# Optimization experiments

Measured on AMD Instinct MI355X. Metric: run time of the kernel, lower is better.

The kernel has to match this reference:

```python
import jax, jax.numpy as jnp
from jax import lax
import numpy as np

B, C, T = 32, 62, 1024
SR = 256
NUM_T = 32
POOL, STEP = 16, 4
OUT_G, POOL_G = 64, 32
NUM_CLASS = 4
KS = [int(0.1 * SR), int(0.2 * SR), int(0.5 * SR)]  # 25, 51, 128
EPS = 1e-30

def _feat_size():
    total = 0
    for k in KS:
        L = T - k + 1
        total += (L - POOL) // STEP + 1
    return NUM_T * (total // 2)  # AvgPool(1,2) halves the concat length

F_DIM = _feat_size()  # 32 * 354 = 11328


def setup_inputs() -> dict:
    key = jax.random.key(0)
    ks = jax.random.split(key, 32)
    n = lambda i, shape, s=0.05: jax.random.normal(ks[i], shape, dtype=jnp.float32) * s
    return dict(
        x=jax.random.normal(ks[0], (B, 1, C, T), dtype=jnp.float32),
        conv1_w=n(1, (NUM_T, 1, 1, KS[0])), conv1_b=jnp.zeros((NUM_T,), jnp.float32),
        conv2_w=n(2, (NUM_T, 1, 1, KS[1])), conv2_b=jnp.zeros((NUM_T,), jnp.float32),
        conv3_w=n(3, (NUM_T, 1, 1, KS[2])), conv3_b=jnp.zeros((NUM_T,), jnp.float32),
        oxo_w=n(4, (NUM_T, NUM_T)), oxo_b=jnp.zeros((NUM_T,), jnp.float32),
        lf_w=n(5, (C, F_DIM), 1.0), lf_b=jnp.zeros((1, C, 1), jnp.float32),
        global_adj=n(6, (C, C), 1.0),
        entry_w=n(7, (F_DIM, OUT_G)), entry_b=jnp.zeros((1, 1, OUT_G), jnp.float32),
        pool_w=n(8, (F_DIM, POOL_G)), pool_b=jnp.zeros((1, 1, POOL_G), jnp.float32),
        pl_w=n(9, (POOL_G, POOL_G), 0.1), pl_b=jnp.zeros((POOL_G,), jnp.float32),
        embed_w=n(10, (OUT_G, OUT_G), 0.1), embed_b=jnp.zeros((1, 1, OUT_G), jnp.float32),
        fc1_w=n(11, (2 * OUT_G, 2 * OUT_G), 0.1), fc1_b=jnp.zeros((2 * OUT_G,), jnp.float32),
        fc2_w=n(12, (2 * OUT_G, OUT_G), 0.1), fc2_b=jnp.zeros((OUT_G,), jnp.float32),
        fc3_w=n(13, (OUT_G, NUM_CLASS), 0.1), fc3_b=jnp.zeros((NUM_CLASS,), jnp.float32),
    )


def _bn(t, axes, eps=1e-5):
    # training-mode batchnorm with gamma=1, beta=0 (init values)
    m = t.mean(axes, keepdims=True)
    v = t.var(axes, keepdims=True)
    return (t - m) / jnp.sqrt(v + eps)


def _temporal(x, w, b):
    # Conv2d(1, NUM_T, (1,k)) -> square -> AvgPool(1,POOL) stride (1,STEP) -> log
    y = lax.conv_general_dilated(x, w, (1, 1), 'VALID',
                                 dimension_numbers=('NCHW', 'OIHW', 'NCHW'))
    y = y + b[None, :, None, None]
    y = y * y
    y = lax.reduce_window(y, 0.0, lax.add, (1, 1, 1, POOL), (1, 1, 1, STEP), 'VALID') / POOL
    return jnp.log(y)


def _forward(x, conv1_w, conv1_b, conv2_w, conv2_b, conv3_w, conv3_b, oxo_w, oxo_b,
             lf_w, lf_b, global_adj, entry_w, entry_b, pool_w, pool_b, pl_w, pl_b,
             embed_w, embed_b, fc1_w, fc1_b, fc2_w, fc2_b, fc3_w, fc3_b):
    # temporal branches, concat along time
    out = jnp.concatenate([_temporal(x, conv1_w, conv1_b),
                           _temporal(x, conv2_w, conv2_b),
                           _temporal(x, conv3_w, conv3_b)], axis=-1)  # [B,NUM_T,C,Lt]
    out = _bn(out, (0, 2, 3))  # BN_t
    # OneXOneConv: dropout(eval)=id, 1x1 conv, leaky_relu, AvgPool(1,2)
    out = jnp.einsum('bchw,oc->bohw', out, oxo_w) + oxo_b[None, :, None, None]
    out = jnp.where(out > 0, out, 0.01 * out)
    out = lax.reduce_window(out, 0.0, lax.add, (1, 1, 1, 2), (1, 1, 1, 2), 'VALID') / 2.0
    out = _bn(out, (0, 2, 3))  # BN_t_
    # [B,NUM_T,C,L] -> [B,C,NUM_T*L]
    out = jnp.transpose(out, (0, 2, 1, 3)).reshape(out.shape[0], C, -1)
    # local_filter_fun + apply_bn
    out = jax.nn.relu(out * lf_w[None] - lf_b)
    out = _bn(out, (0, 2))
    # get_adj: self-similarity, learned global adj, self loops, sym normalization
    s = jnp.einsum('bnf,bmf->bnm', out, out)
    adj = jax.nn.relu(s * (global_adj + global_adj.T)) + jnp.eye(C, dtype=out.dtype)
    rowsum = adj.sum(-1)
    rowsum = jnp.where(rowsum == 0, rowsum + 1.0, rowsum)
    d = rowsum ** -0.5
    adj = adj * d[:, :, None] * d[:, None, :]
    # entry GCN + bn_ + attention pooling (softmax over last dim of size 1 -> ones)
    h_entry = _bn(jnp.einsum('bnm,bmf->bnf', adj, out) @ entry_w - entry_b, (0, 2))
    tg1 = jnp.tanh(h_entry.mean(1))
    sc1 = jax.nn.softmax(jnp.einsum('bnf,bf->bn', h_entry, tg1)[..., None], axis=-1)
    rep1 = jnp.einsum('bnf,bn->bf', h_entry, sc1[..., 0])
    # pool GCN -> assignment
    h_pool = _bn(jnp.einsum('bnm,bmf->bnf', adj, out) @ pool_w - pool_b, (0, 2))
    s_assign = jax.nn.softmax(h_pool @ pl_w + pl_b, axis=-1)  # [B,C,POOL_G]
    # dense_diff_pool
    x_pool = jnp.einsum('bnk,bnf->bkf', s_assign, h_entry)
    adj_pool = jnp.einsum('bnk,bnm,bml->bkl', s_assign, adj, s_assign)
    link = adj - jnp.einsum('bnk,bmk->bnm', s_assign, s_assign) + EPS
    link_loss = jnp.linalg.norm(link.reshape(-1)) / adj.size
    ent_loss = (-s_assign * jnp.log(s_assign + EPS)).sum(-1).mean()
    # embed GCN + apply_bn + attention pooling
    h = _bn(jnp.einsum('bkl,blf->bkf', adj_pool, x_pool) @ embed_w - embed_b, (0, 2))
    tg2 = jnp.tanh(h.mean(1))
    sc2 = jax.nn.softmax(jnp.einsum('bkf,bf->bk', h, tg2)[..., None], axis=-1)
    rep2 = jnp.einsum('bkf,bk->bf', h, sc2[..., 0])
    # head
    o = jnp.concatenate([rep1, rep2], axis=1)
    o = jax.nn.relu(o @ fc1_w + fc1_b)
    o = jax.nn.relu(o @ fc2_w + fc2_b)
    o = o @ fc3_w + fc3_b
    o = _bn(o, (0,))  # apply_bn on [B, num_class]
    return o, link_loss, ent_loss


def reference(x, conv1_w, conv1_b, conv2_w, conv2_b, conv3_w, conv3_b, oxo_w, oxo_b,
              lf_w, lf_b, global_adj, entry_w, entry_b, pool_w, pool_b, pl_w, pl_b,
              embed_w, embed_b, fc1_w, fc1_b, fc2_w, fc2_b, fc3_w, fc3_b):
    return _forward(x, conv1_w, conv1_b, conv2_w, conv2_b, conv3_w, conv3_b, oxo_w, oxo_b,
                    lf_w, lf_b, global_adj, entry_w, entry_b, pool_w, pool_b, pl_w, pl_b,
                    embed_w, embed_b, fc1_w, fc1_b, fc2_w, fc2_b, fc3_w, fc3_b)
```

## Files before the change

### kernel.cpp

```cpp
#include <hip/hip_runtime.h>
#include <math.h>

typedef float  f32x4 __attribute__((ext_vector_type(4)));
typedef short  s16x4 __attribute__((ext_vector_type(4)));
typedef short  s16x8 __attribute__((ext_vector_type(8)));

constexpr int cB  = 32;
constexpr int cC  = 62;
constexpr int cT  = 1024;
constexpr int cNT = 32;
constexpr int cLT = 708;
constexpr int cLT2= 354;
constexpr int cFD = 11328;
constexpr int cNBC = cB*cC;

constexpr size_t FEAT_N = (size_t)cB*cNT*cC*cLT;
constexpr size_t P_N    = (size_t)cB*cC*cC;
constexpr size_t Q_N    = (size_t)cB*cC*96;
constexpr size_t R_N    = (size_t)cB*64;
constexpr size_t PART_N = (size_t)cNBC*64;
constexpr size_t ADJ_N  = P_N;
constexpr size_t HE_N   = (size_t)cB*cC*64;
constexpr size_t HP_N   = (size_t)cB*cC*32;
constexpr size_t HPRE_N = (size_t)cB*32*64;
constexpr int WBF_N = 32*32 + 32*64 + 32*128;
constexpr size_t WT_N = (size_t)96*cFD;

__device__ __forceinline__ unsigned short bf16rne(float v){
  unsigned int u = __float_as_uint(v);
  unsigned int r = (u + 0x7fffu + ((u>>16)&1u)) >> 16;
  return (unsigned short)r;
}

__global__ __launch_bounds__(256) void k_prep(
    const float* __restrict__ w1, const float* __restrict__ w2,
    const float* __restrict__ w3, const float* __restrict__ entry_w,
    const float* __restrict__ pool_w,
    unsigned short* __restrict__ wH, unsigned short* __restrict__ wL,
    float* __restrict__ wcol,
    unsigned short* __restrict__ WTH, unsigned short* __restrict__ WTL)
{
  int blk = blockIdx.x, tid = threadIdx.x;
  if (blk < 28){
    int i = blk*256 + tid;
    float v;
    if (i < 1024){ int f=i>>5, k=i&31; v = (k<25) ? w1[f*25+k] : 0.f; }
    else if (i < 3072){ int j=i-1024; int f=j>>6, k=j&63; v = (k<51) ? w2[f*51+k] : 0.f; }
    else { v = w3[i-3072]; }
    unsigned short h = bf16rne(v);
    float hf = __uint_as_float(((unsigned int)h)<<16);
    wH[i] = h;
    wL[i] = bf16rne(v - hf);
  } else {
    int j = blk - 28;
    float s = 0.f;
    for (int k=tid;k<cFD;k+=256){
      float v = (j<64) ? entry_w[(size_t)k*64 + j] : pool_w[(size_t)k*32 + (j-64)];
      s += v;
      unsigned short h = bf16rne(v);
      float hf = __uint_as_float(((unsigned int)h)<<16);
      WTH[(size_t)j*cFD + k] = h;
      WTL[(size_t)j*cFD + k] = bf16rne(v - hf);
    }
    __shared__ float red[256];
    red[tid]=s; __syncthreads();
    for (int o=128;o>0;o>>=1){ if(tid<o) red[tid]+=red[tid+o]; __syncthreads(); }
    if (tid==0) wcol[j] = red[0];
  }
}

template<int KS, int MT, int WOFF>
__device__ __forceinline__ void mfma_branch(
    const unsigned short* xH, const unsigned short* xL,
    const unsigned short* __restrict__ wHg, const unsigned short* __restrict__ wLg,
    const float* __restrict__ biasg, float* pt, int tid)
{
  int lane = tid & 63, wv = tid >> 6;
  int f = lane & 15, q = lane >> 4;
  int s = lane & 3;
  int a12 = lane & 12;
  s16x8 BH[2][KS], BL[2][KS];
  #pragma unroll
  for (int nt=0; nt<2; nt++)
    #pragma unroll
    for (int ks=0; ks<KS; ks++){
      size_t wo = (size_t)WOFF + (size_t)(nt*16+f)*(KS*32) + ks*32 + q*8;
      BH[nt][ks] = *(const s16x8*)&wHg[wo];
      BL[nt][ks] = *(const s16x8*)&wLg[wo];
    }
  float bv0 = biasg[f], bv1 = biasg[16+f];
  for (int mt = wv; mt < MT; mt += 4){
    f32x4 acc0 = {0.f,0.f,0.f,0.f};
    f32x4 acc1 = {0.f,0.f,0.f,0.f};
    int e0 = mt*16 + a12;
    #pragma unroll
    for (int ks=0; ks<KS; ks++){
      int e = e0 + q*8 + ks*32;
      const unsigned short* ph = xH + s*1160 + e;
      const unsigned short* pl = xL + s*1160 + e;
      s16x4 h0 = *(const s16x4*)ph;
      s16x4 h1 = *(const s16x4*)(ph+4);
      s16x4 l0 = *(const s16x4*)pl;
      s16x4 l1 = *(const s16x4*)(pl+4);
      s16x8 Ah = __builtin_shufflevector(h0,h1,0,1,2,3,4,5,6,7);
      s16x8 Al = __builtin_shufflevector(l0,l1,0,1,2,3,4,5,6,7);
      acc0 = __builtin_amdgcn_mfma_f32_16x16x32_bf16(Ah, BH[0][ks], acc0, 0,0,0);
      acc0 = __builtin_amdgcn_mfma_f32_16x16x32_bf16(Ah, BL[0][ks], acc0, 0,0,0);
      acc0 = __builtin_amdgcn_mfma_f32_16x16x32_bf16(Al, BH[0][ks], acc0, 0,0,0);
      acc1 = __builtin_amdgcn_mfma_f32_16x16x32_bf16(Ah, BH[1][ks], acc1, 0,0,0);
      acc1 = __builtin_amdgcn_mfma_f32_16x16x32_bf16(Ah, BL[1][ks], acc1, 0,0,0);
      acc1 = __builtin_amdgcn_mfma_f32_16x16x32_bf16(Al, BH[1][ks], acc1, 0,0,0);
    }
    float p0=0.f, p1=0.f;
    #pragma unroll
    for (int r=0;r<4;r++){
      float t0 = acc0[r]+bv0; p0 = fmaf(t0,t0,p0);
      float t1 = acc1[r]+bv1; p1 = fmaf(t1,t1,p1);
    }
    pt[(size_t)f*261      + mt*4 + q] = p0;
    pt[(size_t)(16+f)*261 + mt*4 + q] = p1;
  }
}

template<int P, int OFF>
__device__ __forceinline__ void pool_phase(
    const float* pt, float* __restrict__ feat, size_t rstr, size_t base_bc,
    float* tsum, float* tsq, int tid)
{
  bool act = tid < P;
  for (int fi=0; fi<32; fi++){
    float lv = 0.f;
    if (act){
      const float* pp = &pt[(size_t)fi*261 + tid];
      float pooled = (pp[0]+pp[1]+pp[2]+pp[3])*(1.f/16.f);
      lv = __logf(pooled);
      feat[base_bc + (size_t)fi*rstr + OFF + tid] = lv;
    }
    float v = lv, qq = lv*lv;
    #pragma unroll
    for (int o=32;o>0;o>>=1){ v += __shfl_down(v,o,64); qq += __shfl_down(qq,o,64); }
    if ((tid&63)==0){ atomicAdd(&tsum[fi], v); atomicAdd(&tsq[fi], qq); }
  }
}

__global__ __launch_bounds__(256) void k_conv(
    const float* __restrict__ x,
    const unsigned short* __restrict__ wH, const unsigned short* __restrict__ wL,
    const float* __restrict__ b1, const float* __restrict__ b2, const float* __restrict__ b3,
    float* __restrict__ feat, float* __restrict__ part1)
{
  __shared__ unsigned short xH[4*1160];
  __shared__ unsigned short xL[4*1160];
  __shared__ float pt[32*261];
  __shared__ float tsum[32], tsq[32];
  int b = blockIdx.x / cC, c = blockIdx.x % cC;
  int tid = threadIdx.x;
  const float* xg = x + (size_t)(b*cC+c)*cT;
  if (tid<32){ tsum[tid]=0.f; tsq[tid]=0.f; }
  for (int i=tid; i<4*1160; i+=256){
    int s = i / 1160, idx = i - s*1160;
    int src = idx + s;
    float v = (src < 1024) ? xg[src] : 0.f;
    unsigned short h = bf16rne(v);
    float hf = __uint_as_float(((unsigned int)h)<<16);
    xH[i] = h;
    xL[i] = bf16rne(v - hf);
  }
  size_t base_bc = ((size_t)(b*cNT)*cC + c)*cLT;
  size_t rstr = (size_t)cC*cLT;
  __syncthreads();
  mfma_branch<1,63,0>(xH,xL,wH,wL,b1,pt,tid);
  __syncthreads();
  pool_phase<247,0>(pt,feat,rstr,base_bc,tsum,tsq,tid);
  __syncthreads();
  mfma_branch<2,61,1024>(xH,xL,wH,wL,b2,pt,tid);
  __syncthreads();
  pool_phase<240,247>(pt,feat,rstr,base_bc,tsum,tsq,tid);
  __syncthreads();
  mfma_branch<4,57,3072>(xH,xL,wH,wL,b3,pt,tid);
  __syncthreads();
  pool_phase<221,487>(pt,feat,rstr,base_bc,tsum,tsq,tid);
  __syncthreads();
  if (tid<32){
    part1[(size_t)blockIdx.x*64 + tid*2]   = tsum[tid];
    part1[(size_t)blockIdx.x*64 + tid*2+1] = tsq[tid];
  }
}

__global__ __launch_bounds__(256) void k_reduce_stats(
    const float* __restrict__ part, double* __restrict__ stat, int nblk, int nch)
{
  int ch = blockIdx.x, tid = threadIdx.x;
  double s=0,q=0;
  for (int i=tid;i<nblk;i+=256){
    s += (double)part[(size_t)i*nch*2 + ch*2];
    q += (double)part[(size_t)i*nch*2 + ch*2 + 1];
  }
  __shared__ double ls[256], lq[256];
  ls[tid]=s; lq[tid]=q; __syncthreads();
  for (int o=128;o>0;o>>=1){ if(tid<o){ls[tid]+=ls[tid+o]; lq[tid]+=lq[tid+o];} __syncthreads(); }
  if (tid==0){ stat[ch*2]=ls[0]; stat[ch*2+1]=lq[0]; }
}

__global__ void k_foldw(const double* __restrict__ stat1,
                        const float* __restrict__ oxo_w, const float* __restrict__ oxo_b,
                        float* __restrict__ W2T, float* __restrict__ Cf)
{
  __shared__ float mu[32], inv[32];
  int tid = threadIdx.x;
  if (tid<32){
    double cnt = (double)cB*cC*cLT;
    double m = stat1[tid*2]/cnt;
    double v = stat1[tid*2+1]/cnt - m*m;
    mu[tid] = (float)m; inv[tid] = (float)(1.0/sqrt(v+1e-5));
  }
  __syncthreads();
  for (int i=tid;i<1024;i+=256){
    int t=i>>5, o=i&31;
    W2T[t*32+o] = oxo_w[o*32+t]*inv[t];
  }
  if (tid<32){
    float cacc = oxo_b[tid];
    for (int t=0;t<32;t++) cacc -= oxo_w[tid*32+t]*inv[t]*mu[t];
    Cf[tid] = cacc;
  }
}

__global__ __launch_bounds__(256) void k_mix(
    float* __restrict__ feat, const float* __restrict__ W2T,
    const float* __restrict__ Cf, float* __restrict__ part2)
{
  __shared__ float ft[32*240];
  __shared__ float wLh[1024];
  __shared__ float cL[32];
  int b = blockIdx.x / cC, c = blockIdx.x % cC;
  int tid = threadIdx.x;
  int lane = tid & 63, oset = (tid>>6)*8;
  for (int i=tid;i<1024;i+=256) wLh[i] = W2T[i];
  if (tid<32) cL[tid] = Cf[tid];
  float sacc[8]={0,0,0,0,0,0,0,0}, qacc[8]={0,0,0,0,0,0,0,0};
  for (int ch=0; ch<3; ch++){
    int l0 = ch*236;
    __syncthreads();
    for (int g=tid; g<32*59; g+=256){
      int t = g/59, l4 = (g - t*59)*4;
      *(float4*)&ft[t*240+l4] = *(const float4*)&feat[((size_t)(b*cNT+t)*cC + c)*cLT + l0 + l4];
    }
    __syncthreads();
    if (lane < 59){
      float m[8][4];
      #pragma unroll
      for (int f=0;f<8;f++){ float cv=cL[oset+f]; m[f][0]=cv;m[f][1]=cv;m[f][2]=cv;m[f][3]=cv; }
      #pragma unroll 4
      for (int t=0;t<32;t++){
        float4 z = *(const float4*)&ft[t*240 + 4*lane];
        float4 wa = *(const float4*)&wLh[t*32+oset];
        float4 wb = *(const float4*)&wLh[t*32+oset+4];
        float w8a[8] = {wa.x,wa.y,wa.z,wa.w, wb.x,wb.y,wb.z,wb.w};
        #pragma unroll
        for (int f=0;f<8;f++){
          m[f][0]=fmaf(z.x,w8a[f],m[f][0]);
          m[f][1]=fmaf(z.y,w8a[f],m[f][1]);
          m[f][2]=fmaf(z.z,w8a[f],m[f][2]);
          m[f][3]=fmaf(z.w,w8a[f],m[f][3]);
        }
      }
      #pragma unroll
      for (int f=0;f<8;f++){
        float a0 = m[f][0]>0.f ? m[f][0] : 0.01f*m[f][0];
        float a1 = m[f][1]>0.f ? m[f][1] : 0.01f*m[f][1];
        float a2 = m[f][2]>0.f ? m[f][2] : 0.01f*m[f][2];
        float a3 = m[f][3]>0.f ? m[f][3] : 0.01f*m[f][3];
        float v0 = 0.5f*(a0+a1), v1 = 0.5f*(a2+a3);
        float2 st; st.x=v0; st.y=v1;
        *(float2*)&feat[((size_t)(b*cNT+oset+f)*cC + c)*cLT + 118*ch + 2*lane] = st;
        sacc[f] += v0+v1; qacc[f] += v0*v0+v1*v1;
      }
    }
  }
  #pragma unroll
  for (int f=0;f<8;f++){
    float s = sacc[f], q = qacc[f];
    #pragma unroll
    for (int o=32;o>0;o>>=1){ s += __shfl_down(s,o,64); q += __shfl_down(q,o,64); }
    if (lane==0){
      part2[(size_t)blockIdx.x*64 + (oset+f)*2]   = s;
      part2[(size_t)blockIdx.x*64 + (oset+f)*2+1] = q;
    }
  }
}

__global__ __launch_bounds__(256) void k_vprep(
    float* __restrict__ feat, const double* __restrict__ stat2,
    const float* __restrict__ lf_w, const float* __restrict__ lf_b,
    float* __restrict__ r_g, float* __restrict__ SQb)
{
  __shared__ float a_s[32], b_s[32];
  __shared__ float red[256], red2[256];
  int b = blockIdx.x / cC, c = blockIdx.x % cC;
  int tid = threadIdx.x;
  if (tid<32){
    double cnt = (double)cB*cC*cLT2;
    double m = stat2[tid*2]/cnt;
    double v = stat2[tid*2+1]/cnt - m*m;
    float inv = (float)(1.0/sqrt(v+1e-5));
    a_s[tid] = inv;
    b_s[tid] = -(float)m*inv;
  }
  __syncthreads();
  float lb = lf_b[c];
  float S=0.f, SQ=0.f;
  unsigned* featU = (unsigned*)feat;
  for (int i=tid;i<cFD;i+=256){
    int t = i/cLT2, l2 = i - t*cLT2;
    size_t ad = ((size_t)(b*cNT+t)*cC + c)*cLT + l2;
    float raw = feat[ad];
    float z = fmaf(raw, a_s[t], b_s[t]);
    float v = fmaxf(fmaf(z, lf_w[(size_t)c*cFD + i], -lb), 0.f);
    S += v; SQ = fmaf(v,v,SQ);
    unsigned short h = bf16rne(v);
    float hf = __uint_as_float(((unsigned int)h)<<16);
    unsigned short lo = bf16rne(v - hf);
    featU[ad] = (((unsigned)h)<<16) | (unsigned)lo;
  }
  red[tid]=S; red2[tid]=SQ; __syncthreads();
  for (int o=128;o>0;o>>=1){ if(tid<o){red[tid]+=red[tid+o]; red2[tid]+=red2[tid+o];} __syncthreads(); }
  if (tid==0){ r_g[b*64+c]=red[0]; SQb[b*64+c]=red2[0]; }
}

__global__ __launch_bounds__(256) void k_gram(
    const unsigned* __restrict__ featP,
    const unsigned short* __restrict__ WTH, const unsigned short* __restrict__ WTL,
    float* __restrict__ P, float* __restrict__ Q)
{
  __shared__ unsigned short VH[64*72];
  __shared__ unsigned short VL[64*72];
  __shared__ unsigned short WH[96*72];
  __shared__ unsigned short WL[96*72];
  int b = blockIdx.x >> 4, ks = blockIdx.x & 15;
  int tid = threadIdx.x;
  int lane = tid & 63, wv = tid >> 6;
  int cn = lane & 15, q = lane >> 4;
  int nts[3]; int nnt = 0;
  for (int t = wv; t < 10; t += 4) nts[nnt++] = t;
  f32x4 acc[4][3];
  #pragma unroll
  for (int mt=0;mt<4;mt++)
    #pragma unroll
    for (int j=0;j<3;j++) acc[mt][j] = (f32x4){0.f,0.f,0.f,0.f};

  int t0 = (ks*64)/cLT2;
  int l20 = ks*64 - t0*cLT2;
  for (int chunk = ks; chunk < 177; chunk += 16){
    __syncthreads();
    for (int i=tid; i<62*64; i+=256){
      int n = i>>6, k = i&63;
      int fl = l20 + k;
      int cross = (fl >= cLT2);
      int t = t0 + cross;
      int l2 = fl - (cross ? cLT2 : 0);
      unsigned w = featP[((size_t)(b*cNT+t)*cC + n)*cLT + l2];
      VH[n*72+k] = (unsigned short)(w>>16);
      VL[n*72+k] = (unsigned short)(w & 0xffffu);
    }
    {
      int k0 = chunk*64;
      for (int i=tid; i<96*64; i+=256){
        int n = i>>6, k = i&63;
        WH[n*72+k] = WTH[(size_t)n*cFD + k0 + k];
        WL[n*72+k] = WTL[(size_t)n*cFD + k0 + k];
      }
    }
    __syncthreads();
    #pragma unroll
    for (int kst=0;kst<2;kst++){
      s16x8 AH[4], AL[4];
      #pragma unroll
      for (int mt=0;mt<4;mt++){
        AH[mt] = *(const s16x8*)&VH[(mt*16+cn)*72 + kst*32 + q*8];
        AL[mt] = *(const s16x8*)&VL[(mt*16+cn)*72 + kst*32 + q*8];
      }
      for (int j=0;j<nnt;j++){
        int nt = nts[j];
        s16x8 BH, BL;
        if (nt < 4){
          BH = *(const s16x8*)&VH[(nt*16+cn)*72 + kst*32 + q*8];
          BL = *(const s16x8*)&VL[(nt*16+cn)*72 + kst*32 + q*8];
        } else {
          BH = *(const s16x8*)&WH[((nt-4)*16+cn)*72 + kst*32 + q*8];
          BL = *(const s16x8*)&WL[((nt-4)*16+cn)*72 + kst*32 + q*8];
        }
        #pragma unroll
        for (int mt=0;mt<4;mt++){
          acc[mt][j] = __builtin_amdgcn_mfma_f32_16x16x32_bf16(AH[mt], BH, acc[mt][j],0,0,0);
          acc[mt][j] = __builtin_amdgcn_mfma_f32_16x16x32_bf16(AH[mt], BL, acc[mt][j],0,0,0);
          acc[mt][j] = __builtin_amdgcn_mfma_f32_16x16x32_bf16(AL[mt], BH, acc[mt][j],0,0,0);
        }
      }
    }
    l20 += 1024;
    while (l20 >= cLT2){ l20 -= cLT2; t0++; }
  }
  for (int j=0;j<nnt;j++){
    int nt = nts[j];
    for (int mt=0;mt<4;mt++){
      #pragma unroll
      for (int r=0;r<4;r++){
        int m = mt*16 + q*4 + r;
        if (m >= 62) continue;
        float v = acc[mt][j][r];
        if (nt < 4){
          int n = nt*16 + cn;
          if (n < 62) atomicAdd(&P[((size_t)b*cC+m)*cC + n], v);
        } else {
          int jn = (nt-4)*16 + cn;
          atomicAdd(&Q[((size_t)b*cC+m)*96 + jn], v);
        }
      }
    }
  }
}

__global__ __launch_bounds__(256) void k_adjgcn(
    const float* __restrict__ P, const float* __restrict__ r_g,
    const float* __restrict__ SQb,
    const float* __restrict__ gadj, const float* __restrict__ Q,
    const float* __restrict__ wcol,
    const float* __restrict__ entry_b, const float* __restrict__ pool_b,
    float* __restrict__ adj, float* __restrict__ hE, float* __restrict__ hP,
    double* __restrict__ statE, double* __restrict__ statP)
{
  __shared__ float a[3844];
  __shared__ float oL[5952];
  __shared__ float dsh[62];
  __shared__ float rL[62], mL[62], iL[62], wcL[96];
  __shared__ float es[62], eq[62], ps[62], pq[62];
  int b = blockIdx.x, tid = threadIdx.x;
  if (tid<62){
    double S=0, SQ=0;
    for (int b2=0;b2<32;b2++){
      S  += (double)r_g[(size_t)b2*64 + tid];
      SQ += (double)SQb[(size_t)b2*64 + tid];
    }
    double cnt = (double)cB*cFD;
    double m = S/cnt, var = SQ/cnt - m*m;
    mL[tid] = (float)m;
    iL[tid] = (float)(1.0/sqrt(var+1e-5));
    rL[tid] = r_g[(size_t)b*64+tid];
    es[tid]=0.f; eq[tid]=0.f; ps[tid]=0.f; pq[tid]=0.f;
  }
  if (tid>=64 && tid<160) wcL[tid-64]=wcol[tid-64];
  __syncthreads();
  for (int i=tid;i<3844;i+=256){
    int n=i/62, m=i-n*62;
    float sv = (P[(size_t)b*3844+i] - mL[n]*rL[m] - mL[m]*rL[n] + (float)cFD*mL[n]*mL[m]) * iL[n]*iL[m];
    float g = gadj[n*62+m] + gadj[m*62+n];
    float v = sv*g;
    v = v>0.f ? v : 0.f;
    if (n==m) v += 1.f;
    a[i]=v;
  }
  for (int i=tid;i<5952;i+=256){
    int m=i/96, j=i-m*96;
    oL[i] = (Q[(size_t)b*5952+i] - mL[m]*wcL[j]) * iL[m];
  }
  __syncthreads();
  if (tid<62){
    float rsum=0.f;
    for (int m=0;m<62;m++) rsum += a[tid*62+m];
    if (rsum==0.f) rsum=1.f;
    dsh[tid] = 1.0f/sqrtf(rsum);
  }
  __syncthreads();
  for (int i=tid;i<3844;i+=256){
    int n=i/62, m=i-n*62;
    float v = a[i]*dsh[n]*dsh[m];
    a[i] = v;
    adj[(size_t)b*3844+i] = v;
  }
  __syncthreads();
  for (int i=tid;i<5952;i+=256){
    int n=i/96, j=i-n*96;
    float v=0.f;
    for (int m=0;m<62;m++) v = fmaf(a[n*62+m], oL[m*96+j], v);
    if (j<64){
      v -= entry_b[j];
      hE[((size_t)b*62+n)*64 + j] = v;
      atomicAdd(&es[n],v); atomicAdd(&eq[n],v*v);
    } else {
      int j2=j-64;
      v -= pool_b[j2];
      hP[((size_t)b*62+n)*32 + j2] = v;
      atomicAdd(&ps[n],v); atomicAdd(&pq[n],v*v);
    }
  }
  __syncthreads();
  if (tid<62){
    atomicAdd(&statE[tid*2],(double)es[tid]);
    atomicAdd(&statE[tid*2+1],(double)eq[tid]);
    atomicAdd(&statP[tid*2],(double)ps[tid]);
    atomicAdd(&statP[tid*2+1],(double)pq[tid]);
  }
}

__global__ __launch_bounds__(256) void k_pool(
    const float* __restrict__ adj, const float* __restrict__ hEraw,
    const float* __restrict__ hPraw,
    const double* __restrict__ statE, const double* __restrict__ statP,
    const float* __restrict__ pl_w, const float* __restrict__ pl_b,
    const float* __restrict__ embed_w, const float* __restrict__ embed_b,
    float* __restrict__ hpre, double* __restrict__ statH, double* __restrict__ accs)
{
  __shared__ float aL[3844];
  __shared__ float sL[1984];
  __shared__ float hL[3968];
  __shared__ float t1[1984];
  __shared__ float xp[2048];
  __shared__ float ap[1024];
  __shared__ float red[256];
  __shared__ float ksum[32], ksq[32];
  __shared__ float mE[62], iE[62], mP[62], iP[62];
  float* e1 = hL;
  float* sT = t1;
  float* hPL = xp;
  float* plw = ap;
  int b = blockIdx.x, tid = threadIdx.x;
  if (tid<62){
    double cntE = (double)cB*64;
    double m = statE[tid*2]/cntE;
    double v = statE[tid*2+1]/cntE - m*m;
    mE[tid]=(float)m; iE[tid]=(float)(1.0/sqrt(v+1e-5));
    double cntP = (double)cB*32;
    double m2 = statP[tid*2]/cntP;
    double v2 = statP[tid*2+1]/cntP - m2*m2;
    mP[tid]=(float)m2; iP[tid]=(float)(1.0/sqrt(v2+1e-5));
  }
  if (tid<32){ksum[tid]=0.f;ksq[tid]=0.f;}
  for (int i=tid;i<3844;i+=256) aL[i]=adj[(size_t)b*3844+i];
  for (int i=tid;i<1984;i+=256) hPL[i]=hPraw[(size_t)b*1984+i];
  for (int i=tid;i<1024;i+=256) plw[i]=pl_w[i];
  __syncthreads();
  for (int i=tid;i<3968;i+=256){
    int n = i>>6;
    hL[i] = (hEraw[(size_t)b*3968+i]-mE[n])*iE[n];
  }
  int r0 = tid>>5, o = tid&31;
  float entacc = 0.f;
  for (int n=r0; n<62; n+=8){
    float y = pl_b[o];
    float mm = mP[n], ii = iP[n];
    #pragma unroll 8
    for (int j=0;j<32;j++)
      y = fmaf((hPL[n*32+j]-mm)*ii, plw[j*32+o], y);
    float mx = y;
    for (int d=16;d>0;d>>=1) mx = fmaxf(mx, __shfl_xor(mx,d,32));
    float e = expf(y-mx);
    float sum = e;
    for (int d=16;d>0;d>>=1) sum += __shfl_xor(sum,d,32);
    float p = e/sum;
    sL[n*32+o] = p;
    entacc += -p*logf(p+1e-30f);
  }
  red[tid]=entacc; __syncthreads();
  for (int o2=128;o2>0;o2>>=1){ if(tid<o2) red[tid]+=red[tid+o2]; __syncthreads(); }
  if (tid==0) atomicAdd(&accs[1], (double)red[0]);
  __syncthreads();
  for (int i=tid;i<2048;i+=256){
    int k=i>>6, f=i&63;
    float v=0.f;
    for (int n=0;n<62;n++) v = fmaf(sL[n*32+k], hL[n*64+f], v);
    xp[i]=v;
  }
  for (int i=tid;i<1984;i+=256){
    int n=i>>5, k=i&31;
    float v=0.f;
    for (int m=0;m<62;m++) v = fmaf(aL[n*62+m], sL[m*32+k], v);
    t1[i]=v;
  }
  __syncthreads();
  for (int i=tid;i<1024;i+=256){
    int k=i>>5, l=i&31;
    float v=0.f;
    for (int n=0;n<62;n++) v = fmaf(sL[n*32+k], t1[n*32+l], v);
    ap[i]=v;
  }
  __syncthreads();
  for (int i=tid;i<1984;i+=256){
    int k=i/62, n=i-k*62;
    sT[k*62+n] = sL[n*32+k];
  }
  __syncthreads();
  float lacc=0.f;
  for (int i=tid;i<3844;i+=256){
    int n=i/62, m=i-n*62;
    float v=0.f;
    for (int k=0;k<32;k++) v = fmaf(sT[k*62+n], sT[k*62+m], v);
    float d = aL[i]-v+1e-30f;
    lacc = fmaf(d,d,lacc);
  }
  red[tid]=lacc; __syncthreads();
  for (int o2=128;o2>0;o2>>=1){ if(tid<o2) red[tid]+=red[tid+o2]; __syncthreads(); }
  if (tid==0) atomicAdd(&accs[0], (double)red[0]);
  __syncthreads();
  for (int i=tid;i<2048;i+=256){
    int k=i>>6, f=i&63;
    float v=0.f;
    for (int l=0;l<32;l++) v = fmaf(ap[k*32+l], xp[l*64+f], v);
    e1[i]=v;
  }
  __syncthreads();
  for (int i=tid;i<2048;i+=256){
    int k=i>>6, j=i&63;
    float v=0.f;
    for (int f=0;f<64;f++) v = fmaf(e1[k*64+f], embed_w[f*64+j], v);
    v -= embed_b[j];
    hpre[(size_t)b*2048 + i] = v;
    atomicAdd(&ksum[k], v);
    atomicAdd(&ksq[k], v*v);
  }
  __syncthreads();
  if (tid<32){
    atomicAdd(&statH[tid*2],   (double)ksum[tid]);
    atomicAdd(&statH[tid*2+1], (double)ksq[tid]);
  }
}

__global__ __launch_bounds__(128) void k_head(
    const float* __restrict__ hEraw, const float* __restrict__ hpre,
    const double* __restrict__ statE, const double* __restrict__ statH,
    const float* __restrict__ fc1_w, const float* __restrict__ fc1_b,
    const float* __restrict__ fc2_w, const float* __restrict__ fc2_b,
    const float* __restrict__ fc3_w, const float* __restrict__ fc3_b,
    float* __restrict__ o_pre)
{
  __shared__ float o1[128], y1[128], y2[64];
  __shared__ float mk[32], ik[32];
  __shared__ float mE[62], iE[62];
  int b = blockIdx.x, tid = threadIdx.x;
  if (tid<32){
    double cnt = 2048.0;
    double m = statH[tid*2]/cnt;
    double v = statH[tid*2+1]/cnt - m*m;
    mk[tid]=(float)m; ik[tid]=(float)(1.0/sqrt(v+1e-5));
  }
  if (tid>=64 && tid<126){
    int n = tid-64;
    double cnt = (double)cB*64;
    double m = statE[n*2]/cnt;
    double v = statE[n*2+1]/cnt - m*m;
    mE[n]=(float)m; iE[n]=(float)(1.0/sqrt(v+1e-5));
  }
  __syncthreads();
  if (tid<64){
    float s1=0.f;
    for (int n=0;n<62;n++)
      s1 += (hEraw[((size_t)b*62+n)*64+tid]-mE[n])*iE[n];
    o1[tid]=s1;
    float s2=0.f;
    for (int k=0;k<32;k++) s2 += (hpre[(size_t)b*2048 + k*64+tid]-mk[k])*ik[k];
    o1[64+tid]=s2;
  }
  __syncthreads();
  {
    float y = fc1_b[tid];
    for (int j=0;j<128;j++) y = fmaf(o1[j], fc1_w[j*128+tid], y);
    y1[tid] = fmaxf(y,0.f);
  }
  __syncthreads();
  if (tid<64){
    float z = fc2_b[tid];
    for (int j=0;j<128;j++) z = fmaf(y1[j], fc2_w[j*64+tid], z);
    y2[tid]=fmaxf(z,0.f);
  }
  __syncthreads();
  if (tid<4){
    float w = fc3_b[tid];
    for (int j=0;j<64;j++) w = fmaf(y2[j], fc3_w[j*4+tid], w);
    o_pre[b*4+tid]=w;
  }
}

__global__ void k_final(const float* __restrict__ o_pre, const double* __restrict__ accs,
                        float* __restrict__ out)
{
  int tid = threadIdx.x;
  if (tid<4){
    float s=0.f,q=0.f;
    for (int b=0;b<32;b++){ float v=o_pre[b*4+tid]; s+=v; q+=v*v; }
    float m = s*(1.f/32.f);
    float var = q*(1.f/32.f) - m*m;
    float inv = 1.0f/sqrtf(var+1e-5f);
    for (int b=0;b<32;b++) out[b*4+tid] = (o_pre[b*4+tid]-m)*inv;
  }
  if (tid==4) out[128] = (float)(sqrt(accs[0])/123008.0);
  if (tid==5) out[129] = (float)(accs[1]/1984.0);
}

__global__ void k_wsfail(float* __restrict__ out, int n)
{
  int i = blockIdx.x*256 + threadIdx.x;
  if (i < n) out[i] = 12345.0f;
}

extern "C" void kernel_launch(void* const* d_in, const int* in_sizes, int n_in,
                              void* d_out, int out_size, void* d_ws, size_t ws_size,
                              hipStream_t stream)
{
  const float* x       = (const float*)d_in[0];
  const float* w1      = (const float*)d_in[1];
  const float* b1      = (const float*)d_in[2];
  const float* w2      = (const float*)d_in[3];
  const float* b2      = (const float*)d_in[4];
  const float* w3      = (const float*)d_in[5];
  const float* b3      = (const float*)d_in[6];
  const float* oxo_w   = (const float*)d_in[7];
  const float* oxo_b   = (const float*)d_in[8];
  const float* lf_w    = (const float*)d_in[9];
  const float* lf_b    = (const float*)d_in[10];
  const float* gadj    = (const float*)d_in[11];
  const float* entry_w = (const float*)d_in[12];
  const float* entry_b = (const float*)d_in[13];
  const float* pool_w  = (const float*)d_in[14];
  const float* pool_b  = (const float*)d_in[15];
  const float* pl_w    = (const float*)d_in[16];
  const float* pl_b    = (const float*)d_in[17];
  const float* embed_w = (const float*)d_in[18];
  const float* embed_b = (const float*)d_in[19];
  const float* fc1_w   = (const float*)d_in[20];
  const float* fc1_b   = (const float*)d_in[21];
  const float* fc2_w   = (const float*)d_in[22];
  const float* fc2_b   = (const float*)d_in[23];
  const float* fc3_w   = (const float*)d_in[24];
  const float* fc3_b   = (const float*)d_in[25];

  char* ws = (char*)d_ws;
  size_t off = 0;
  auto take = [&](size_t bytes){ size_t o = off; off = (off + bytes + 15) & ~(size_t)15; return o; };

  size_t feat_o = take(FEAT_N*4);
  size_t zstart = off;
  size_t P_o     = take(P_N*4);
  size_t Q_o     = take(Q_N*4);
  size_t r_o     = take(R_N*4);
  size_t sqb_o   = take(R_N*4);
  size_t statE_o = take(124*8);
  size_t statP_o = take(124*8);
  size_t statH_o = take(64*8);
  size_t accs_o  = take(2*8);
  size_t zend = off;
  size_t stat1_o = take(64*8);
  size_t stat2_o = take(64*8);
  size_t wcol_o  = take(96*4);
  size_t w2t_o   = take(1024*4);
  size_t cf_o    = take(32*4);
  size_t part1_o = take(PART_N*4);
  size_t part2_o = take(PART_N*4);
  size_t adj_o   = take(ADJ_N*4);
  size_t hE_o    = take(HE_N*4);
  size_t hP_o    = take(HP_N*4);
  size_t hpre_o  = take(HPRE_N*4);
  size_t opre_o  = take(128*4);
  size_t wbfH_o  = take(WBF_N*2);
  size_t wbfL_o  = take(WBF_N*2);
  size_t wtH_o   = take(WT_N*2);
  size_t wtL_o   = take(WT_N*2);

  if (off > ws_size) {
    k_wsfail<<<(out_size+255)/256, 256, 0, stream>>>((float*)d_out, out_size);
    return;
  }

  float*  feat  = (float*)(ws+feat_o);
  float*  P_g   = (float*)(ws+P_o);
  float*  Q_g   = (float*)(ws+Q_o);
  float*  r_g   = (float*)(ws+r_o);
  float*  SQb   = (float*)(ws+sqb_o);
  double* statE = (double*)(ws+statE_o);
  double* statP = (double*)(ws+statP_o);
  double* statH = (double*)(ws+statH_o);
  double* accs  = (double*)(ws+accs_o);
  double* stat1 = (double*)(ws+stat1_o);
  double* stat2 = (double*)(ws+stat2_o);
  float*  wcol  = (float*)(ws+wcol_o);
  float*  W2T   = (float*)(ws+w2t_o);
  float*  Cf    = (float*)(ws+cf_o);
  float*  part1 = (float*)(ws+part1_o);
  float*  part2 = (float*)(ws+part2_o);
  float*  adj_g = (float*)(ws+adj_o);
  float*  hE_g  = (float*)(ws+hE_o);
  float*  hP_g  = (float*)(ws+hP_o);
  float*  hpre  = (float*)(ws+hpre_o);
  float*  opre  = (float*)(ws+opre_o);
  unsigned short* wbfH = (unsigned short*)(ws+wbfH_o);
  unsigned short* wbfL = (unsigned short*)(ws+wbfL_o);
  unsigned short* WTH  = (unsigned short*)(ws+wtH_o);
  unsigned short* WTL  = (unsigned short*)(ws+wtL_o);
  float*  out   = (float*)d_out;

  hipMemsetAsync(ws + zstart, 0, zend - zstart, stream);

  k_prep<<<124, 256, 0, stream>>>(w1, w2, w3, entry_w, pool_w, wbfH, wbfL, wcol, WTH, WTL);
  k_conv<<<cNBC, 256, 0, stream>>>(x, wbfH, wbfL, b1, b2, b3, feat, part1);
  k_reduce_stats<<<32, 256, 0, stream>>>(part1, stat1, cNBC, 32);
  k_foldw<<<1, 256, 0, stream>>>(stat1, oxo_w, oxo_b, W2T, Cf);
  k_mix<<<cNBC, 256, 0, stream>>>(feat, W2T, Cf, part2);
  k_reduce_stats<<<32, 256, 0, stream>>>(part2, stat2, cNBC, 32);
  k_vprep<<<cNBC, 256, 0, stream>>>(feat, stat2, lf_w, lf_b, r_g, SQb);
  k_gram<<<cB*16, 256, 0, stream>>>((const unsigned*)feat, WTH, WTL, P_g, Q_g);
  k_adjgcn<<<cB, 256, 0, stream>>>(P_g, r_g, SQb, gadj, Q_g, wcol, entry_b, pool_b,
                                   adj_g, hE_g, hP_g, statE, statP);
  k_pool<<<cB, 256, 0, stream>>>(adj_g, hE_g, hP_g, statE, statP, pl_w, pl_b,
                                 embed_w, embed_b, hpre, statH, accs);
  k_head<<<cB, 128, 0, stream>>>(hE_g, hpre, statE, statH, fc1_w, fc1_b, fc2_w, fc2_b, fc3_w, fc3_b, opre);
  k_final<<<1, 64, 0, stream>>>(opre, accs, out);
}
```

Baseline: 757.4 us.

## Recompute normalized features in gram kernel and drop packed write-back; wave-split pool phase

The vprep kernel no longer writes bf16 hi/lo packed features back to global memory. It becomes a read-only statistics kernel, and the gram kernel recomputes the batchnorm, lf_w scaling and ReLU on the fly while staging tiles into shared memory. This removes one full write pass over the large feature tensor but makes the gram kernel redo the elementwise transform and read lf_w. Separately, pool_phase now gives each wave 8 filters and has lane 0 add into the shared sums directly, replacing per-filter shared-memory atomics across all waves.

```diff
diff --git a/kernel.cpp b/kernel.cpp
--- a/kernel.cpp
+++ b/kernel.cpp
@@ -127,19 +127,25 @@
     const float* pt, float* __restrict__ feat, size_t rstr, size_t base_bc,
     float* tsum, float* tsq, int tid)
 {
-  bool act = tid < P;
-  for (int fi=0; fi<32; fi++){
-    float lv = 0.f;
-    if (act){
-      const float* pp = &pt[(size_t)fi*261 + tid];
-      float pooled = (pp[0]+pp[1]+pp[2]+pp[3])*(1.f/16.f);
-      lv = __logf(pooled);
-      feat[base_bc + (size_t)fi*rstr + OFF + tid] = lv;
-    }
-    float v = lv, qq = lv*lv;
+  int lane = tid & 63, wv = tid >> 6;
+  #pragma unroll
+  for (int f8=0; f8<8; f8++){
+    int fi = wv*8 + f8;
+    float val=0.f, vsq=0.f;
     #pragma unroll
-    for (int o=32;o>0;o>>=1){ v += __shfl_down(v,o,64); qq += __shfl_down(qq,o,64); }
-    if ((tid&63)==0){ atomicAdd(&tsum[fi], v); atomicAdd(&tsq[fi], qq); }
+    for (int ch=0; ch<4; ch++){
+      int p = ch*64 + lane;
+      if (p < P){
+        const float* pp = &pt[(size_t)fi*261 + p];
+        float pooled = (pp[0]+pp[1]+pp[2]+pp[3])*(1.f/16.f);
+        float lv = __logf(pooled);
+        feat[base_bc + (size_t)fi*rstr + OFF + p] = lv;
+        val += lv; vsq += lv*lv;
+      }
+    }
+    #pragma unroll
+    for (int o=32;o>0;o>>=1){ val += __shfl_down(val,o,64); vsq += __shfl_down(vsq,o,64); }
+    if (lane==0){ tsum[fi] += val; tsq[fi] += vsq; }
   }
 }
 
@@ -290,8 +296,8 @@
   }
 }
 
-__global__ __launch_bounds__(256) void k_vprep(
-    float* __restrict__ feat, const double* __restrict__ stat2,
+__global__ __launch_bounds__(256) void k_vstat(
+    const float* __restrict__ feat, const double* __restrict__ stat2,
     const float* __restrict__ lf_w, const float* __restrict__ lf_b,
     float* __restrict__ r_g, float* __restrict__ SQb)
 {
@@ -310,18 +316,12 @@
   __syncthreads();
   float lb = lf_b[c];
   float S=0.f, SQ=0.f;
-  unsigned* featU = (unsigned*)feat;
   for (int i=tid;i<cFD;i+=256){
     int t = i/cLT2, l2 = i - t*cLT2;
-    size_t ad = ((size_t)(b*cNT+t)*cC + c)*cLT + l2;
-    float raw = feat[ad];
+    float raw = feat[((size_t)(b*cNT+t)*cC + c)*cLT + l2];
     float z = fmaf(raw, a_s[t], b_s[t]);
     float v = fmaxf(fmaf(z, lf_w[(size_t)c*cFD + i], -lb), 0.f);
     S += v; SQ = fmaf(v,v,SQ);
-    unsigned short h = bf16rne(v);
-    float hf = __uint_as_float(((unsigned int)h)<<16);
-    unsigned short lo = bf16rne(v - hf);
-    featU[ad] = (((unsigned)h)<<16) | (unsigned)lo;
   }
   red[tid]=S; red2[tid]=SQ; __syncthreads();
   for (int o=128;o>0;o>>=1){ if(tid<o){red[tid]+=red[tid+o]; red2[tid]+=red2[tid+o];} __syncthreads(); }
@@ -329,7 +329,8 @@
 }
 
 __global__ __launch_bounds__(256) void k_gram(
-    const unsigned* __restrict__ featP,
+    const float* __restrict__ feat, const double* __restrict__ stat2,
+    const float* __restrict__ lf_w, const float* __restrict__ lf_b,
     const unsigned short* __restrict__ WTH, const unsigned short* __restrict__ WTL,
     float* __restrict__ P, float* __restrict__ Q)
 {
@@ -337,10 +338,20 @@
   __shared__ unsigned short VL[64*72];
   __shared__ unsigned short WH[96*72];
   __shared__ unsigned short WL[96*72];
+  __shared__ float a_s[32], b_s[32], lbs[64];
   int b = blockIdx.x >> 4, ks = blockIdx.x & 15;
   int tid = threadIdx.x;
   int lane = tid & 63, wv = tid >> 6;
   int cn = lane & 15, q = lane >> 4;
+  if (tid<32){
+    double cnt = (double)cB*cC*cLT2;
+    double m = stat2[tid*2]/cnt;
+    double v = stat2[tid*2+1]/cnt - m*m;
+    float inv = (float)(1.0/sqrt(v+1e-5));
+    a_s[tid] = inv;
+    b_s[tid] = -(float)m*inv;
+  }
+  if (tid>=64 && tid<128) lbs[tid-64] = (tid-64<62) ? lf_b[tid-64] : 0.f;
   int nts[3]; int nnt = 0;
   for (int t = wv; t < 10; t += 4) nts[nnt++] = t;
   f32x4 acc[4][3];
@@ -352,6 +363,7 @@
   int t0 = (ks*64)/cLT2;
   int l20 = ks*64 - t0*cLT2;
   for (int chunk = ks; chunk < 177; chunk += 16){
+    int k0 = chunk*64;
     __syncthreads();
     for (int i=tid; i<62*64; i+=256){
       int n = i>>6, k = i&63;
@@ -359,17 +371,18 @@
       int cross = (fl >= cLT2);
       int t = t0 + cross;
       int l2 = fl - (cross ? cLT2 : 0);
-      unsigned w = featP[((size_t)(b*cNT+t)*cC + n)*cLT + l2];
-      VH[n*72+k] = (unsigned short)(w>>16);
-      VL[n*72+k] = (unsigned short)(w & 0xffffu);
-    }
-    {
-      int k0 = chunk*64;
-      for (int i=tid; i<96*64; i+=256){
-        int n = i>>6, k = i&63;
-        WH[n*72+k] = WTH[(size_t)n*cFD + k0 + k];
-        WL[n*72+k] = WTL[(size_t)n*cFD + k0 + k];
-      }
+      float raw = feat[((size_t)(b*cNT+t)*cC + n)*cLT + l2];
+      float z = fmaf(raw, a_s[t], b_s[t]);
+      float v = fmaxf(fmaf(z, lf_w[(size_t)n*cFD + k0 + k], -lbs[n]), 0.f);
+      unsigned short h = bf16rne(v);
+      float hf = __uint_as_float(((unsigned int)h)<<16);
+      VH[n*72+k] = h;
+      VL[n*72+k] = bf16rne(v - hf);
+    }
+    for (int i=tid; i<96*64; i+=256){
+      int n = i>>6, k = i&63;
+      WH[n*72+k] = WTH[(size_t)n*cFD + k0 + k];
+      WL[n*72+k] = WTL[(size_t)n*cFD + k0 + k];
     }
     __syncthreads();
     #pragma unroll
@@ -741,13 +754,13 @@
   size_t zstart = off;
   size_t P_o     = take(P_N*4);
   size_t Q_o     = take(Q_N*4);
-  size_t r_o     = take(R_N*4);
-  size_t sqb_o   = take(R_N*4);
   size_t statE_o = take(124*8);
   size_t statP_o = take(124*8);
   size_t statH_o = take(64*8);
   size_t accs_o  = take(2*8);
   size_t zend = off;
+  size_t r_o     = take(R_N*4);
+  size_t sqb_o   = take(R_N*4);
   size_t stat1_o = take(64*8);
   size_t stat2_o = take(64*8);
   size_t wcol_o  = take(96*4);
@@ -805,8 +818,8 @@
   k_foldw<<<1, 256, 0, stream>>>(stat1, oxo_w, oxo_b, W2T, Cf);
   k_mix<<<cNBC, 256, 0, stream>>>(feat, W2T, Cf, part2);
   k_reduce_stats<<<32, 256, 0, stream>>>(part2, stat2, cNBC, 32);
-  k_vprep<<<cNBC, 256, 0, stream>>>(feat, stat2, lf_w, lf_b, r_g, SQb);
-  k_gram<<<cB*16, 256, 0, stream>>>((const unsigned*)feat, WTH, WTL, P_g, Q_g);
+  k_vstat<<<cNBC, 256, 0, stream>>>(feat, stat2, lf_w, lf_b, r_g, SQb);
+  k_gram<<<cB*16, 256, 0, stream>>>(feat, stat2, lf_w, lf_b, WTH, WTL, P_g, Q_g);
   k_adjgcn<<<cB, 256, 0, stream>>>(P_g, r_g, SQb, gadj, Q_g, wcol, entry_b, pool_b,
                                    adj_g, hE_g, hP_g, statE, statP);
   k_pool<<<cB, 256, 0, stream>>>(adj_g, hE_g, hP_g, statE, statP, pl_w, pl_b,
```

Measured after the change: 653.5 us. 13.7% less time.
